# Kernel tuning notes

Hardware: AMD Instinct MI355X
Metric: run time of the kernel (lower is better)

Reference implementation:

```python
import jax, jax.numpy as jnp
import numpy as np

N = 100000
E = 1600000
D_IN = 128
K = 2
D_OUT = 128


def setup_inputs() -> dict:
    key = jax.random.key(0)
    k1, k2, k3, k4, k5, k6 = jax.random.split(key, 6)
    x = jax.random.normal(k1, (N, D_IN), dtype=jnp.float32)
    edge_src = jax.random.randint(k2, (E,), 0, N, dtype=jnp.int32)  # row indices of sparse adj
    edge_dst = jax.random.randint(k3, (E,), 0, N, dtype=jnp.int32)  # col indices of sparse adj
    edge_val = jax.random.uniform(k4, (E,), dtype=jnp.float32)
    # Linear(in_features*(k+1), out_features), xavier_normal with relu gain
    fan_in = D_IN * (K + 1)
    gain = np.sqrt(2.0)  # calculate_gain('relu')
    std = gain * np.sqrt(2.0 / (fan_in + D_OUT))
    W = jax.random.normal(k5, (D_OUT, fan_in), dtype=jnp.float32) * std
    b = jax.random.uniform(k6, (D_OUT,), dtype=jnp.float32, minval=-1.0, maxval=1.0) / np.sqrt(fan_in)
    return {"x": x, "edge_src": edge_src, "edge_dst": edge_dst, "edge_val": edge_val, "W": W, "b": b}


def _spmm(edge_src, edge_dst, edge_val, feat):
    # y[i] = sum_{e: src[e]==i} val[e] * feat[dst[e]]
    msgs = edge_val[:, None] * feat[edge_dst]  # [E, D]
    return jax.ops.segment_sum(msgs, edge_src, num_segments=N)


def reference(x, edge_src, edge_dst, edge_val, W, b):
    fstack = [x]
    for _ in range(K):
        fstack.append(_spmm(edge_src, edge_dst, edge_val, fstack[-1]))
    h = jnp.concatenate(fstack, axis=-1)  # [N, D_IN*(K+1)]
    out = h @ W.T + b  # [N, D_OUT]
    # norm=False, activation=None, dropout=False per init defaults
    return out
```

## Files before the change

kernel.cpp:

```cpp
#include <hip/hip_runtime.h>
#include <hip/hip_bf16.h>

#define NN 100000
#define EE 1600000
#define D 128
#define BKT 391
#define CAP 5120

typedef __attribute__((ext_vector_type(4))) float f32x4;
typedef __attribute__((ext_vector_type(8))) short s16x8;

__device__ inline ushort f2bf(float f) {
    uint b = __float_as_uint(f);
    return (ushort)((b + 0x7fffu + ((b >> 16) & 1u)) >> 16);
}
__device__ inline float bflo(uint g) { return __uint_as_float(g << 16); }
__device__ inline float bfhi(uint g) { return __uint_as_float(g & 0xffff0000u); }

__global__ __launch_bounds__(256) void cvt_bf16(
    const float* __restrict__ in, ushort* __restrict__ out, int n4)
{
    const int i = blockIdx.x * 256 + threadIdx.x;
    if (i >= n4) return;
    const float4 v = reinterpret_cast<const float4*>(in)[i];
    ushort4 o;
    o.x = f2bf(v.x); o.y = f2bf(v.y); o.z = f2bf(v.z); o.w = f2bf(v.w);
    reinterpret_cast<ushort4*>(out)[i] = o;
}

__global__ __launch_bounds__(256) void bucket_pass1(
    const int* __restrict__ src, const int* __restrict__ dst,
    const float* __restrict__ val, int* __restrict__ cursor,
    int2* __restrict__ barr)
{
    __shared__ int    cnt[BKT];
    __shared__ int    lbase[BKT];
    __shared__ int    gbase[BKT];
    __shared__ int    tmp[256];
    __shared__ int2   staged[2048];
    __shared__ ushort bkt_of[2048];
    const int t = threadIdx.x;
    for (int u = t; u < BKT; u += 256) cnt[u] = 0;
    __syncthreads();

    int ebk[8], erk[8]; int2 epk[8];
    const int e0 = blockIdx.x * 2048 + t;
    #pragma unroll
    for (int it = 0; it < 8; ++it) {
        const int e = e0 + it * 256;
        ebk[it] = -1;
        if (e < EE) {
            const int s = src[e];
            const int bk = s >> 8;
            ebk[it] = bk;
            erk[it] = atomicAdd(&cnt[bk], 1);
            epk[it] = make_int2(__float_as_int(val[e]), dst[e] | ((s & 255) << 17));
        }
    }
    __syncthreads();

    {
        const int i0 = 2 * t, i1 = 2 * t + 1;
        const int c0 = (i0 < BKT) ? cnt[i0] : 0;
        const int c1 = (i1 < BKT) ? cnt[i1] : 0;
        const int s = c0 + c1;
        tmp[t] = s;
        __syncthreads();
        for (int off = 1; off < 256; off <<= 1) {
            const int v = (t >= off) ? tmp[t - off] : 0;
            __syncthreads();
            tmp[t] += v;
            __syncthreads();
        }
        const int excl = tmp[t] - s;
        if (i0 < BKT) lbase[i0] = excl;
        if (i1 < BKT) lbase[i1] = excl + c0;
    }
    for (int u = t; u < BKT; u += 256)
        gbase[u] = (cnt[u] > 0) ? atomicAdd(&cursor[u], cnt[u]) : 0;
    __syncthreads();

    #pragma unroll
    for (int it = 0; it < 8; ++it) {
        if (ebk[it] >= 0) {
            const int pos = lbase[ebk[it]] + erk[it];
            staged[pos] = epk[it];
            bkt_of[pos] = (ushort)ebk[it];
        }
    }
    __syncthreads();

    const int total = min(2048, EE - blockIdx.x * 2048);
    for (int i = t; i < total; i += 256) {
        const int bk = bkt_of[i];
        barr[(size_t)bk * CAP + gbase[bk] + (i - lbase[bk])] = staged[i];
    }
}

__global__ __launch_bounds__(512) void scan_buckets(
    const int* __restrict__ cursor, int* __restrict__ bbase, int* __restrict__ rp)
{
    __shared__ int tmp[512];
    const int t = threadIdx.x;
    const int s = (t < BKT) ? cursor[t] : 0;
    tmp[t] = s;
    __syncthreads();
    for (int off = 1; off < 512; off <<= 1) {
        const int v = (t >= off) ? tmp[t - off] : 0;
        __syncthreads();
        tmp[t] += v;
        __syncthreads();
    }
    if (t < BKT) bbase[t] = tmp[t] - s;
    if (t == BKT - 1) bbase[BKT] = tmp[t];
    if (t == 0) rp[NN] = EE;
}

__global__ __launch_bounds__(256) void bucket_pass2(
    const int* __restrict__ bbase, const int2* __restrict__ barr,
    int* __restrict__ rp, int2* __restrict__ csr)
{
    __shared__ int rowcnt[256];
    __shared__ int tmp[256];
    __shared__ int rowcur[256];
    __shared__ int2 sorted[CAP];
    const int b = blockIdx.x;
    const int t = threadIdx.x;
    const int gb = bbase[b];
    const int sz = bbase[b + 1] - gb;
    const int2* my = barr + (size_t)b * CAP;

    rowcnt[t] = 0;
    __syncthreads();
    for (int i = t; i < sz; i += 256)
        atomicAdd(&rowcnt[(my[i].y >> 17) & 255], 1);
    __syncthreads();
    const int c = rowcnt[t];
    tmp[t] = c;
    __syncthreads();
    for (int off = 1; off < 256; off <<= 1) {
        const int v = (t >= off) ? tmp[t - off] : 0;
        __syncthreads();
        tmp[t] += v;
        __syncthreads();
    }
    const int excl = tmp[t] - c;
    rowcur[t] = excl;
    const int row = b * 256 + t;
    if (row < NN) rp[row] = gb + excl;
    __syncthreads();
    for (int i = t; i < sz; i += 256) {
        const int2 e = my[i];
        const int rl = (e.y >> 17) & 255;
        const int slot = atomicAdd(&rowcur[rl], 1);
        sorted[slot] = make_int2(e.y & 0x1FFFF, e.x);
    }
    __syncthreads();
    for (int i = t; i < sz; i += 256)
        csr[gb + i] = sorted[i];
}

__global__ __launch_bounds__(256) void spmm_csr_bf16(
    const int* __restrict__ rp, const int2* __restrict__ csr,
    const ushort* __restrict__ featb, ushort* __restrict__ outb)
{
    const int tid  = blockIdx.x * 256 + threadIdx.x;
    const int row  = tid >> 6;
    const int lane = threadIdx.x & 63;
    const int g    = lane >> 4;
    const int li   = lane & 15;

    const int start = rp[row];
    const int end   = rp[row + 1];

    float acc[8] = {0.f, 0.f, 0.f, 0.f, 0.f, 0.f, 0.f, 0.f};

    for (int base = start; base < end; base += 16) {
        #pragma unroll
        for (int k = 0; k < 4; ++k) {
            const int p  = base + k * 4 + g;
            const int pc = (p < end) ? p : start;
            const int2 e = csr[pc];
            const float v = (p < end) ? __int_as_float(e.y) : 0.f;
            const uint4 gg = *reinterpret_cast<const uint4*>(featb + (size_t)e.x * 128 + li * 8);
            acc[0] = fmaf(v, bflo(gg.x), acc[0]); acc[1] = fmaf(v, bfhi(gg.x), acc[1]);
            acc[2] = fmaf(v, bflo(gg.y), acc[2]); acc[3] = fmaf(v, bfhi(gg.y), acc[3]);
            acc[4] = fmaf(v, bflo(gg.z), acc[4]); acc[5] = fmaf(v, bfhi(gg.z), acc[5]);
            acc[6] = fmaf(v, bflo(gg.w), acc[6]); acc[7] = fmaf(v, bfhi(gg.w), acc[7]);
        }
    }

    #pragma unroll
    for (int i = 0; i < 8; ++i) {
        acc[i] += __shfl_xor(acc[i], 16);
        acc[i] += __shfl_xor(acc[i], 32);
    }

    if (g == 0) {
        uint4 o;
        o.x = ((uint)f2bf(acc[1]) << 16) | (uint)f2bf(acc[0]);
        o.y = ((uint)f2bf(acc[3]) << 16) | (uint)f2bf(acc[2]);
        o.z = ((uint)f2bf(acc[5]) << 16) | (uint)f2bf(acc[4]);
        o.w = ((uint)f2bf(acc[7]) << 16) | (uint)f2bf(acc[6]);
        *reinterpret_cast<uint4*>(outb + (size_t)row * 128 + li * 8) = o;
    }
}

__global__ __launch_bounds__(512) void gemm_mfma(
    const ushort* __restrict__ xb, const ushort* __restrict__ f1b,
    const ushort* __restrict__ f2b, const ushort* __restrict__ Wb,
    const float* __restrict__ b, float* __restrict__ out)
{
    __shared__ ushort Ws[128 * 64];

    const int t    = threadIdx.x;
    const int wave = t >> 6;
    const int lane = t & 63;
    const int lr   = lane & 15;
    const int lg   = lane >> 4;
    const int rbase = blockIdx.x * 128;

    int arow = rbase + wave * 16 + lr;
    if (arow >= NN) arow = NN - 1;

    f32x4 acc[8];
    #pragma unroll
    for (int j = 0; j < 8; ++j) {
        const float bv = b[j * 16 + lr];
        acc[j] = (f32x4){bv, bv, bv, bv};
    }

    for (int c = 0; c < 6; ++c) {
        const ushort* src = (c < 2) ? xb : ((c < 4) ? f1b : f2b);
        const int col0 = (c & 1) * 64;
        const int k0w  = c * 64;

        #pragma unroll
        for (int it = 0; it < 2; ++it) {
            const int idx = it * 512 + t;
            const int col = idx >> 3, seg = idx & 7;
            const s16x8 v = *reinterpret_cast<const s16x8*>(Wb + (size_t)col * 384 + k0w + seg * 8);
            *reinterpret_cast<s16x8*>(&Ws[col * 64 + ((seg ^ (col & 7)) * 8)]) = v;
        }

        const s16x8 a0 = *reinterpret_cast<const s16x8*>(src + (size_t)arow * 128 + col0 + lg * 8);
        const s16x8 a1 = *reinterpret_cast<const s16x8*>(src + (size_t)arow * 128 + col0 + 32 + lg * 8);

        __syncthreads();

        #pragma unroll
        for (int kk = 0; kk < 2; ++kk) {
            const s16x8 a = kk ? a1 : a0;
            #pragma unroll
            for (int j = 0; j < 8; ++j) {
                const int bcol = j * 16 + lr;
                const int bch  = (kk * 4 + lg) ^ (bcol & 7);
                const s16x8 bf = *reinterpret_cast<const s16x8*>(&Ws[bcol * 64 + bch * 8]);
                acc[j] = __builtin_amdgcn_mfma_f32_16x16x32_bf16(a, bf, acc[j], 0, 0, 0);
            }
        }
        __syncthreads();
    }

    #pragma unroll
    for (int j = 0; j < 8; ++j) {
        #pragma unroll
        for (int j2 = 0; j2 < 4; ++j2) {
            const int rg = rbase + wave * 16 + lg * 4 + j2;
            if (rg < NN)
                out[(size_t)rg * 128 + j * 16 + lr] = acc[j][j2];
        }
    }
}

extern "C" void kernel_launch(void* const* d_in, const int* in_sizes, int n_in,
                              void* d_out, int out_size, void* d_ws, size_t ws_size,
                              hipStream_t stream)
{
    const float* x    = (const float*)d_in[0];
    const int*   esrc = (const int*)  d_in[1];
    const int*   edst = (const int*)  d_in[2];
    const float* eval = (const float*)d_in[3];
    const float* W    = (const float*)d_in[4];
    const float* b    = (const float*)d_in[5];
    float* out = (float*)d_out;

    char* ws = (char*)d_ws;
    const size_t FB = (size_t)NN * D * 2;
    ushort* xb     = (ushort*)(ws);
    ushort* f1b    = (ushort*)(ws + FB);
    ushort* f2b    = (ushort*)(ws + 2 * FB);
    ushort* Wb     = (ushort*)(ws + 3 * FB);
    char*   p      = ws + 3 * FB + 98304;
    int2*   csr    = (int2*)p;               p += (size_t)EE * 8;
    int2*   barr   = (int2*)p;               p += (size_t)BKT * CAP * 8;
    int*    cursor = (int*)p;                p += (BKT + 1) * 4;
    int*    bbase  = (int*)p;                p += (BKT + 1) * 4;
    int*    rp     = (int*)p;

    hipMemsetAsync(cursor, 0, BKT * sizeof(int), stream);

    cvt_bf16<<<(NN * D / 4 + 255) / 256, 256, 0, stream>>>(x, xb, NN * D / 4);
    cvt_bf16<<<(128 * 384 / 4 + 255) / 256, 256, 0, stream>>>(W, Wb, 128 * 384 / 4);

    bucket_pass1<<<(EE + 2047) / 2048, 256, 0, stream>>>(esrc, edst, eval, cursor, barr);
    scan_buckets<<<1, 512, 0, stream>>>(cursor, bbase, rp);
    bucket_pass2<<<BKT, 256, 0, stream>>>(bbase, barr, rp, csr);

    spmm_csr_bf16<<<NN / 4, 256, 0, stream>>>(rp, csr, xb,  f1b);
    spmm_csr_bf16<<<NN / 4, 256, 0, stream>>>(rp, csr, f1b, f2b);

    gemm_mfma<<<(NN + 127) / 128, 512, 0, stream>>>(xb, f1b, f2b, Wb, b, out);
}
```

Measured before the change: 315.8 us.

## Fuse conversion kernels, inline bucket scan, enlarge pass1 tiles, restructure SpMM and GEMM loads

Merges the two bf16 conversion launches into one kernel. Removes the separate bucket-scan kernel by having each pass2 block reduce the preceding bucket counts itself. Doubles the edges per bucket_pass1 block to cut global atomics and block count. Also rewrites the SpMM inner loop to process 8 edges per iteration with predicated loads, and hoists all A-fragment loads in the GEMM ahead of the K loop. These reduce launch overhead and expose more memory parallelism, at the cost of higher register and shared-memory use and redundant scan work across blocks.

```diff
diff --git a/kernel.cpp b/kernel.cpp
--- a/kernel.cpp
+++ b/kernel.cpp
@@ -6,6 +6,7 @@
 #define D 128
 #define BKT 391
 #define CAP 5120
+#define P1E 4096
 
 typedef __attribute__((ext_vector_type(4))) float f32x4;
 typedef __attribute__((ext_vector_type(8))) short s16x8;
@@ -17,15 +18,25 @@
 __device__ inline float bflo(uint g) { return __uint_as_float(g << 16); }
 __device__ inline float bfhi(uint g) { return __uint_as_float(g & 0xffff0000u); }
 
-__global__ __launch_bounds__(256) void cvt_bf16(
-    const float* __restrict__ in, ushort* __restrict__ out, int n4)
+#define XN4 (NN * D / 4)
+#define WN4 (128 * 384 / 4)
+__global__ __launch_bounds__(256) void cvt_both(
+    const float* __restrict__ x, ushort* __restrict__ xb,
+    const float* __restrict__ W, ushort* __restrict__ Wb)
 {
     const int i = blockIdx.x * 256 + threadIdx.x;
-    if (i >= n4) return;
-    const float4 v = reinterpret_cast<const float4*>(in)[i];
-    ushort4 o;
-    o.x = f2bf(v.x); o.y = f2bf(v.y); o.z = f2bf(v.z); o.w = f2bf(v.w);
-    reinterpret_cast<ushort4*>(out)[i] = o;
+    if (i < XN4) {
+        const float4 v = reinterpret_cast<const float4*>(x)[i];
+        ushort4 o;
+        o.x = f2bf(v.x); o.y = f2bf(v.y); o.z = f2bf(v.z); o.w = f2bf(v.w);
+        reinterpret_cast<ushort4*>(xb)[i] = o;
+    } else if (i < XN4 + WN4) {
+        const int j = i - XN4;
+        const float4 v = reinterpret_cast<const float4*>(W)[j];
+        ushort4 o;
+        o.x = f2bf(v.x); o.y = f2bf(v.y); o.z = f2bf(v.z); o.w = f2bf(v.w);
+        reinterpret_cast<ushort4*>(Wb)[j] = o;
+    }
 }
 
 __global__ __launch_bounds__(256) void bucket_pass1(
@@ -37,16 +48,16 @@
     __shared__ int    lbase[BKT];
     __shared__ int    gbase[BKT];
     __shared__ int    tmp[256];
-    __shared__ int2   staged[2048];
-    __shared__ ushort bkt_of[2048];
+    __shared__ int2   staged[P1E];
+    __shared__ ushort bkt_of[P1E];
     const int t = threadIdx.x;
     for (int u = t; u < BKT; u += 256) cnt[u] = 0;
     __syncthreads();
 
-    int ebk[8], erk[8]; int2 epk[8];
-    const int e0 = blockIdx.x * 2048 + t;
-    #pragma unroll
-    for (int it = 0; it < 8; ++it) {
+    int ebk[16], erk[16]; int2 epk[16];
+    const int e0 = blockIdx.x * P1E + t;
+    #pragma unroll
+    for (int it = 0; it < 16; ++it) {
         const int e = e0 + it * 256;
         ebk[it] = -1;
         if (e < EE) {
@@ -81,7 +92,7 @@
     __syncthreads();
 
     #pragma unroll
-    for (int it = 0; it < 8; ++it) {
+    for (int it = 0; it < 16; ++it) {
         if (ebk[it] >= 0) {
             const int pos = lbase[ebk[it]] + erk[it];
             staged[pos] = epk[it];
@@ -90,45 +101,40 @@
     }
     __syncthreads();
 
-    const int total = min(2048, EE - blockIdx.x * 2048);
+    const int total = min(P1E, EE - blockIdx.x * P1E);
     for (int i = t; i < total; i += 256) {
         const int bk = bkt_of[i];
         barr[(size_t)bk * CAP + gbase[bk] + (i - lbase[bk])] = staged[i];
     }
 }
 
-__global__ __launch_bounds__(512) void scan_buckets(
-    const int* __restrict__ cursor, int* __restrict__ bbase, int* __restrict__ rp)
-{
-    __shared__ int tmp[512];
-    const int t = threadIdx.x;
-    const int s = (t < BKT) ? cursor[t] : 0;
-    tmp[t] = s;
-    __syncthreads();
-    for (int off = 1; off < 512; off <<= 1) {
-        const int v = (t >= off) ? tmp[t - off] : 0;
-        __syncthreads();
-        tmp[t] += v;
-        __syncthreads();
-    }
-    if (t < BKT) bbase[t] = tmp[t] - s;
-    if (t == BKT - 1) bbase[BKT] = tmp[t];
-    if (t == 0) rp[NN] = EE;
-}
-
 __global__ __launch_bounds__(256) void bucket_pass2(
-    const int* __restrict__ bbase, const int2* __restrict__ barr,
+    const int* __restrict__ cursor, const int2* __restrict__ barr,
     int* __restrict__ rp, int2* __restrict__ csr)
 {
+    __shared__ int tmp[256];
+    __shared__ int gbs;
     __shared__ int rowcnt[256];
-    __shared__ int tmp[256];
     __shared__ int rowcur[256];
     __shared__ int2 sorted[CAP];
     const int b = blockIdx.x;
     const int t = threadIdx.x;
-    const int gb = bbase[b];
-    const int sz = bbase[b + 1] - gb;
+
+    int partial = 0;
+    if (t < b)       partial += cursor[t];
+    if (t + 256 < b) partial += cursor[t + 256];
+    tmp[t] = partial;
+    __syncthreads();
+    for (int off = 128; off > 0; off >>= 1) {
+        if (t < off) tmp[t] += tmp[t + off];
+        __syncthreads();
+    }
+    if (t == 0) gbs = tmp[0];
+    __syncthreads();
+    const int gb = gbs;
+    const int sz = cursor[b];
     const int2* my = barr + (size_t)b * CAP;
+    if (b == BKT - 1 && t == 0) rp[NN] = EE;
 
     rowcnt[t] = 0;
     __syncthreads();
@@ -175,19 +181,24 @@
 
     float acc[8] = {0.f, 0.f, 0.f, 0.f, 0.f, 0.f, 0.f, 0.f};
 
-    for (int base = start; base < end; base += 16) {
-        #pragma unroll
-        for (int k = 0; k < 4; ++k) {
-            const int p  = base + k * 4 + g;
-            const int pc = (p < end) ? p : start;
-            const int2 e = csr[pc];
-            const float v = (p < end) ? __int_as_float(e.y) : 0.f;
-            const uint4 gg = *reinterpret_cast<const uint4*>(featb + (size_t)e.x * 128 + li * 8);
-            acc[0] = fmaf(v, bflo(gg.x), acc[0]); acc[1] = fmaf(v, bfhi(gg.x), acc[1]);
-            acc[2] = fmaf(v, bflo(gg.y), acc[2]); acc[3] = fmaf(v, bfhi(gg.y), acc[3]);
-            acc[4] = fmaf(v, bflo(gg.z), acc[4]); acc[5] = fmaf(v, bfhi(gg.z), acc[5]);
-            acc[6] = fmaf(v, bflo(gg.w), acc[6]); acc[7] = fmaf(v, bfhi(gg.w), acc[7]);
-        }
+    for (int base = start; base < end; base += 8) {
+        const int p0 = base + g;
+        const int p1 = base + 4 + g;
+        int2 e0 = make_int2(0, 0), e1 = make_int2(0, 0);
+        if (p0 < end) e0 = csr[p0];
+        if (p1 < end) e1 = csr[p1];
+        const float v0 = __int_as_float(e0.y);
+        const float v1 = __int_as_float(e1.y);
+        const uint4 g0 = *reinterpret_cast<const uint4*>(featb + (size_t)e0.x * 128 + li * 8);
+        const uint4 g1 = *reinterpret_cast<const uint4*>(featb + (size_t)e1.x * 128 + li * 8);
+        acc[0] = fmaf(v0, bflo(g0.x), acc[0]); acc[1] = fmaf(v0, bfhi(g0.x), acc[1]);
+        acc[2] = fmaf(v0, bflo(g0.y), acc[2]); acc[3] = fmaf(v0, bfhi(g0.y), acc[3]);
+        acc[4] = fmaf(v0, bflo(g0.z), acc[4]); acc[5] = fmaf(v0, bfhi(g0.z), acc[5]);
+        acc[6] = fmaf(v0, bflo(g0.w), acc[6]); acc[7] = fmaf(v0, bfhi(g0.w), acc[7]);
+        acc[0] = fmaf(v1, bflo(g1.x), acc[0]); acc[1] = fmaf(v1, bfhi(g1.x), acc[1]);
+        acc[2] = fmaf(v1, bflo(g1.y), acc[2]); acc[3] = fmaf(v1, bfhi(g1.y), acc[3]);
+        acc[4] = fmaf(v1, bflo(g1.z), acc[4]); acc[5] = fmaf(v1, bfhi(g1.z), acc[5]);
+        acc[6] = fmaf(v1, bflo(g1.w), acc[6]); acc[7] = fmaf(v1, bfhi(g1.w), acc[7]);
     }
 
     #pragma unroll
@@ -223,6 +234,15 @@
     int arow = rbase + wave * 16 + lr;
     if (arow >= NN) arow = NN - 1;
 
+    s16x8 a[6][2];
+    #pragma unroll
+    for (int c = 0; c < 6; ++c) {
+        const ushort* src = (c < 2) ? xb : ((c < 4) ? f1b : f2b);
+        const int col0 = (c & 1) * 64;
+        a[c][0] = *reinterpret_cast<const s16x8*>(src + (size_t)arow * 128 + col0 + lg * 8);
+        a[c][1] = *reinterpret_cast<const s16x8*>(src + (size_t)arow * 128 + col0 + 32 + lg * 8);
+    }
+
     f32x4 acc[8];
     #pragma unroll
     for (int j = 0; j < 8; ++j) {
@@ -230,10 +250,9 @@
         acc[j] = (f32x4){bv, bv, bv, bv};
     }
 
+    #pragma unroll
     for (int c = 0; c < 6; ++c) {
-        const ushort* src = (c < 2) ? xb : ((c < 4) ? f1b : f2b);
-        const int col0 = (c & 1) * 64;
-        const int k0w  = c * 64;
+        const int k0w = c * 64;
 
         #pragma unroll
         for (int it = 0; it < 2; ++it) {
@@ -242,21 +261,16 @@
             const s16x8 v = *reinterpret_cast<const s16x8*>(Wb + (size_t)col * 384 + k0w + seg * 8);
             *reinterpret_cast<s16x8*>(&Ws[col * 64 + ((seg ^ (col & 7)) * 8)]) = v;
         }
-
-        const s16x8 a0 = *reinterpret_cast<const s16x8*>(src + (size_t)arow * 128 + col0 + lg * 8);
-        const s16x8 a1 = *reinterpret_cast<const s16x8*>(src + (size_t)arow * 128 + col0 + 32 + lg * 8);
-
         __syncthreads();
 
         #pragma unroll
         for (int kk = 0; kk < 2; ++kk) {
-            const s16x8 a = kk ? a1 : a0;
             #pragma unroll
             for (int j = 0; j < 8; ++j) {
                 const int bcol = j * 16 + lr;
                 const int bch  = (kk * 4 + lg) ^ (bcol & 7);
                 const s16x8 bf = *reinterpret_cast<const s16x8*>(&Ws[bcol * 64 + bch * 8]);
-                acc[j] = __builtin_amdgcn_mfma_f32_16x16x32_bf16(a, bf, acc[j], 0, 0, 0);
+                acc[j] = __builtin_amdgcn_mfma_f32_16x16x32_bf16(a[c][kk], bf, acc[j], 0, 0, 0);
             }
         }
         __syncthreads();
@@ -295,17 +309,14 @@
     int2*   csr    = (int2*)p;               p += (size_t)EE * 8;
     int2*   barr   = (int2*)p;               p += (size_t)BKT * CAP * 8;
     int*    cursor = (int*)p;                p += (BKT + 1) * 4;
-    int*    bbase  = (int*)p;                p += (BKT + 1) * 4;
     int*    rp     = (int*)p;
 
     hipMemsetAsync(cursor, 0, BKT * sizeof(int), stream);
 
-    cvt_bf16<<<(NN * D / 4 + 255) / 256, 256, 0, stream>>>(x, xb, NN * D / 4);
-    cvt_bf16<<<(128 * 384 / 4 + 255) / 256, 256, 0, stream>>>(W, Wb, 128 * 384 / 4);
-
-    bucket_pass1<<<(EE + 2047) / 2048, 256, 0, stream>>>(esrc, edst, eval, cursor, barr);
-    scan_buckets<<<1, 512, 0, stream>>>(cursor, bbase, rp);
-    bucket_pass2<<<BKT, 256, 0, stream>>>(bbase, barr, rp, csr);
+    cvt_both<<<(XN4 + WN4 + 255) / 256, 256, 0, stream>>>(x, xb, W, Wb);
+
+    bucket_pass1<<<(EE + P1E - 1) / P1E, 256, 0, stream>>>(esrc, edst, eval, cursor, barr);
+    bucket_pass2<<<BKT, 256, 0, stream>>>(cursor, barr, rp, csr);
 
     spmm_csr_bf16<<<NN / 4, 256, 0, stream>>>(rp, csr, xb,  f1b);
     spmm_csr_bf16<<<NN / 4, 256, 0, stream>>>(rp, csr, f1b, f2b);
```

Measured after the change: 311.7 us. No clear change (-1.3%).
